# Performance work log

Measured on AMD Instinct MI355X. Metric: run time of the kernel, lower is better.

## Reference

```python
import jax, jax.numpy as jnp
import numpy as np

N_NODES = 50000
N_EDGES = 1600000
D_FEAT = 128
EMB = 32
HEADS = 4
SLOPE = 0.2  # PyG GATv2 default negative_slope


def setup_inputs() -> dict:
    key = jax.random.key(0)
    ks = jax.random.split(key, 12)
    H, C = HEADS, EMB
    hid = H * C  # concat output dim = 128

    def glorot(k, shape):
        fan_in, fan_out = shape[0], shape[-1] if len(shape) > 1 else shape[0]
        lim = jnp.sqrt(6.0 / (fan_in + fan_out)).astype(jnp.float32)
        return jax.random.uniform(k, shape, jnp.float32, -lim, lim)

    x = jax.random.normal(ks[0], (N_NODES, D_FEAT), jnp.float32)
    edge_index = jax.random.randint(ks[1], (2, N_EDGES), 0, N_NODES, jnp.int32).astype(jnp.int64)

    return {
        "x": x,
        "edge_index": edge_index,
        # layer 1: in D_FEAT -> H*C (separate source/target lins, share_weights=False)
        "W1_l": glorot(ks[2], (D_FEAT, hid)),
        "W1_r": glorot(ks[3], (D_FEAT, hid)),
        "att1": glorot(ks[4], (H, C)),
        "b1": jnp.zeros((hid,), jnp.float32),
        # layer 2: in H*C -> H*C
        "W2_l": glorot(ks[5], (hid, hid)),
        "W2_r": glorot(ks[6], (hid, hid)),
        "att2": glorot(ks[7], (H, C)),
        "b2": jnp.zeros((hid,), jnp.float32),
    }


def _gatv2_layer(x, src, dst, W_l, W_r, att, bias, n_nodes):
    H, C = att.shape
    xl = (x @ W_l).reshape(n_nodes, H, C)  # source-side transform
    xr = (x @ W_r).reshape(n_nodes, H, C)  # target-side transform
    # per-edge pre-activation: GATv2 applies LeakyReLU BEFORE the attention dot
    msg = xl[src] + xr[dst]                               # [E, H, C]
    e = jnp.einsum('ehc,hc->eh', jax.nn.leaky_relu(msg, SLOPE), att)  # [E, H]
    # numerically stable segment softmax over incoming edges of each dst node
    m = jax.ops.segment_max(e, dst, num_segments=n_nodes)  # [N, H]
    ex = jnp.exp(e - m[dst])
    denom = jax.ops.segment_sum(ex, dst, num_segments=n_nodes)  # [N, H]
    alpha = ex / (denom[dst] + 1e-16)                     # [E, H]
    out = jax.ops.segment_sum(alpha[:, :, None] * xl[src], dst, num_segments=n_nodes)
    return out.reshape(n_nodes, H * C) + bias


def reference(x, edge_index, W1_l, W1_r, att1, b1, W2_l, W2_r, att2, b2):
    n = x.shape[0]
    # PyG default add_self_loops=True: append (i -> i) for every node
    loop = jnp.arange(n, dtype=edge_index.dtype)
    src = jnp.concatenate([edge_index[0], loop])
    dst = jnp.concatenate([edge_index[1], loop])
    h = jax.nn.relu(_gatv2_layer(x, src, dst, W1_l, W1_r, att1, b1, n))
    h = jax.nn.relu(_gatv2_layer(h, src, dst, W2_l, W2_r, att2, b2, n))
    return h
```

## Files before the change

### kernel.cpp

```cpp
#include <hip/hip_runtime.h>

#define N_NODES 50000
#define N_EDGES 1600000
#define ET (N_EDGES + N_NODES)
#define DF 128
#define SLOPE 0.2f

#define NB2 391
#define CAP2 6144
#define P1_CHUNK 4096
#define GEMM_BLOCKS ((N_NODES + 63) / 64)
#define BIN_BLOCKS ((ET + P1_CHUNK - 1) / P1_CHUNK)
#define WCONV_BLOCKS 256

typedef __attribute__((ext_vector_type(4))) float floatx4;
typedef __attribute__((ext_vector_type(8))) _Float16 half8;
typedef __attribute__((ext_vector_type(2))) _Float16 half2v;

__device__ __forceinline__ void wconv_body(
    int bid,
    const float* __restrict__ W0, const float* __restrict__ W1,
    const float* __restrict__ W2, const float* __restrict__ W3,
    _Float16* __restrict__ Wh, _Float16* __restrict__ Wl)
{
    int idx = bid * 256 + threadIdx.x;
    int m = idx >> 14, rem = idx & 16383;
    const float* W = (m == 0) ? W0 : (m == 1) ? W1 : (m == 2) ? W2 : W3;
    int c = rem >> 7, k = rem & 127;
    float v = W[k * 128 + c];
    _Float16 h = (_Float16)v;
    int slab = k >> 5, q = (k >> 3) & 3, j = k & 7;
    size_t o = (size_t)m * 16384 + (size_t)((slab << 2) + q) * 1024 + (c << 3) + j;
    Wh[o] = h;
    Wl[o] = (_Float16)(v - (float)h);
}

__device__ __forceinline__ void bin_body(
    int bid, const int* __restrict__ ei,
    int* __restrict__ g_count, int* __restrict__ bucket_mem, char* smem_)
{
    int* cnt  = (int*)smem_;
    int* base = cnt + NB2;
    int* cnt2 = base + NB2;
    const int tid = threadIdx.x;

    for (int i = tid; i < NB2; i += 256) { cnt[i] = 0; cnt2[i] = 0; }
    __syncthreads();

    const int e0 = bid * P1_CHUNK;
    int srcv[16], dstv[16];
#pragma unroll
    for (int i = 0; i < 16; i++) {
        int eid = e0 + i * 256 + tid;
        int s = 0, d = -1;
        if (eid < ET) {
            if (eid < N_EDGES) { s = ei[eid]; d = ei[N_EDGES + eid]; }
            else               { s = d = eid - N_EDGES; }
        }
        srcv[i] = s; dstv[i] = d;
        if (d >= 0) atomicAdd(&cnt[d >> 7], 1);
    }
    __syncthreads();
    for (int i = tid; i < NB2; i += 256)
        base[i] = (cnt[i] > 0) ? atomicAdd(&g_count[i], cnt[i]) : 0;
    __syncthreads();
#pragma unroll
    for (int i = 0; i < 16; i++) {
        int d = dstv[i];
        if (d >= 0) {
            int b = d >> 7;
            int r = atomicAdd(&cnt2[b], 1);
            int slot = base[b] + r;
            if (slot < CAP2)
                bucket_mem[(size_t)b * CAP2 + slot] =
                    (srcv[i] & 0xFFFF) | ((d & 127) << 16);
        }
    }
}

__global__ __launch_bounds__(256) void prep_bin(
    const float* __restrict__ W0, const float* __restrict__ W1,
    const float* __restrict__ W2, const float* __restrict__ W3,
    _Float16* __restrict__ Wh, _Float16* __restrict__ Wl,
    const int* __restrict__ ei,
    int* __restrict__ g_count, int* __restrict__ bucket_mem)
{
    __shared__ char smem[4704];
    if (blockIdx.x < WCONV_BLOCKS)
        wconv_body(blockIdx.x, W0, W1, W2, W3, Wh, Wl);
    else
        bin_body(blockIdx.x - WCONV_BLOCKS, ei, g_count, bucket_mem, smem);
}

__device__ __forceinline__ half8 load_h8(const float* p) {
    float4 a = *(const float4*)(p);
    float4 b = *(const float4*)(p + 4);
    half8 h;
    h[0] = (_Float16)a.x; h[1] = (_Float16)a.y;
    h[2] = (_Float16)a.z; h[3] = (_Float16)a.w;
    h[4] = (_Float16)b.x; h[5] = (_Float16)b.y;
    h[6] = (_Float16)b.z; h[7] = (_Float16)b.w;
    return h;
}
__device__ __forceinline__ half8 load_h8(const _Float16* p) {
    return *(const half8*)p;
}

template<typename T>
__device__ __forceinline__ void gemm_body(
    int bid, const T* __restrict__ X,
    const _Float16* __restrict__ WhL, const _Float16* __restrict__ WlL,
    const _Float16* __restrict__ WhR, const _Float16* __restrict__ WlR,
    _Float16* __restrict__ outL, _Float16* __restrict__ outR, int M, char* smem_)
{
    _Float16* xs  = (_Float16*)smem_;
    _Float16* whL = xs + 64 * 40;
    _Float16* wlL = whL + 4096;
    _Float16* whR = wlL + 4096;
    _Float16* wlR = whR + 4096;

    const int t = threadIdx.x;
    const int row0 = bid * 64;
    const int lane = t & 63, wv = t >> 6;
    const int lm = lane & 15, quad = lane >> 4;
    const int m0 = wv * 16;

    floatx4 accL[8], accR[8];
#pragma unroll
    for (int i = 0; i < 8; i++) { accL[i] = (floatx4)0.f; accR[i] = (floatx4)0.f; }

    const int sr = t >> 2;
    const int sc = (t & 3) * 8;

    for (int kb = 0; kb < 128; kb += 32) {
        const int slab = kb >> 5;
        int xrow = row0 + sr; if (xrow >= M) xrow = M - 1;
        half8 xv = load_h8(X + (size_t)xrow * DF + kb + sc);
        *(half8*)&xs[sr * 40 + sc] = xv;

        {
            const size_t sbase = (size_t)slab * 4096;
            const _Float16* gsrc[4] = { WhL + sbase, WlL + sbase,
                                        WhR + sbase, WlR + sbase };
            _Float16* ldst[4] = { whL, wlL, whR, wlR };
#pragma unroll
            for (int b = 0; b < 4; b++) {
#pragma unroll
                for (int i = 0; i < 2; i++) {
                    const int chunk = wv * 2 + i;
                    const _Float16* src = gsrc[b] + chunk * 512 + lane * 8;
                    __builtin_amdgcn_global_load_lds(
                        (const __attribute__((address_space(1))) void*)src,
                        (__attribute__((address_space(3))) void*)(ldst[b] + chunk * 512),
                        16, 0, 0);
                }
            }
        }
        __syncthreads();

        half8 af = *(const half8*)&xs[(m0 + lm) * 40 + quad * 8];
#pragma unroll
        for (int nt = 0; nt < 8; nt++) {
            const int bofs = quad * 1024 + (nt * 16 + lm) * 8;
            half8 bh = *(const half8*)&whL[bofs];
            half8 bl = *(const half8*)&wlL[bofs];
            accL[nt] = __builtin_amdgcn_mfma_f32_16x16x32_f16(af, bh, accL[nt], 0, 0, 0);
            accL[nt] = __builtin_amdgcn_mfma_f32_16x16x32_f16(af, bl, accL[nt], 0, 0, 0);
            half8 ch = *(const half8*)&whR[bofs];
            half8 cl = *(const half8*)&wlR[bofs];
            accR[nt] = __builtin_amdgcn_mfma_f32_16x16x32_f16(af, ch, accR[nt], 0, 0, 0);
            accR[nt] = __builtin_amdgcn_mfma_f32_16x16x32_f16(af, cl, accR[nt], 0, 0, 0);
        }
        __syncthreads();
    }

#pragma unroll
    for (int nt = 0; nt < 8; nt++) {
        int col = (nt >> 2) * 64 + (nt & 3) * 16 + lm;
#pragma unroll
        for (int r = 0; r < 4; r++) {
            int gr = row0 + m0 + quad * 4 + r;
            if (gr < M) {
                size_t o = (size_t)gr * DF + col;
                outL[o] = (_Float16)accL[nt][r];
                outR[o] = (_Float16)accR[nt][r];
            }
        }
    }
}

__device__ __forceinline__ void csr_body(
    int b, const int* __restrict__ g_count, const int* __restrict__ bucket_mem,
    int* __restrict__ row_ptr, unsigned short* __restrict__ csr_src, char* smem_)
{
    int* sh_edges = (int*)smem_;
    int* hist = sh_edges + 6144;
    int* excl = hist + 128;
    int* cnt2 = excl + 128;
    int* sA   = cnt2 + 128;
    int* sB   = sA + 512;
    const int tid = threadIdx.x;

    sA[tid]       = (tid < NB2)       ? g_count[tid]       : 0;
    sA[tid + 256] = (tid + 256 < NB2) ? g_count[tid + 256] : 0;
    __syncthreads();
    int* in = sA; int* outp = sB;
    for (int d = 1; d < 512; d <<= 1) {
        for (int i = tid; i < 512; i += 256)
            outp[i] = in[i] + ((i >= d) ? in[i - d] : 0);
        __syncthreads();
        int* tmp = in; in = outp; outp = tmp;
    }
    const int base_csr = (b > 0) ? in[b - 1] : 0;

    int m = g_count[b]; if (m > CAP2) m = CAP2;
    if (tid < 128) { hist[tid] = 0; cnt2[tid] = 0; }
    __syncthreads();
    const int* bm = bucket_mem + (size_t)b * CAP2;
    for (int i = tid; i < m; i += 256) {
        int p = bm[i];
        sh_edges[i] = p;
        atomicAdd(&hist[(p >> 16) & 127], 1);
    }
    __syncthreads();
    if (tid < 128) sA[tid] = hist[tid];
    __syncthreads();
    for (int d = 1; d < 128; d <<= 1) {
        int x = 0;
        if (tid < 128 && tid >= d) x = sA[tid - d];
        __syncthreads();
        if (tid < 128) sA[tid] += x;
        __syncthreads();
    }
    if (tid < 128) {
        excl[tid] = sA[tid] - hist[tid];
        int node = (b << 7) + tid;
        if (node < N_NODES) row_ptr[node] = base_csr + excl[tid];
    }
    if (b == 0 && tid == 0) row_ptr[N_NODES] = ET;
    __syncthreads();
    for (int i = tid; i < m; i += 256) {
        int p = sh_edges[i];
        int dl = (p >> 16) & 127;
        int r = atomicAdd(&cnt2[dl], 1);
        csr_src[base_csr + excl[dl] + r] = (unsigned short)(p & 0xFFFF);
    }
}

__global__ __launch_bounds__(256) void gemm_csr(
    const float* __restrict__ X,
    const _Float16* __restrict__ Wh, const _Float16* __restrict__ Wl,
    _Float16* __restrict__ outL, _Float16* __restrict__ outR,
    const int* __restrict__ g_count, const int* __restrict__ bucket_mem,
    int* __restrict__ row_ptr, unsigned short* __restrict__ csr_src)
{
    __shared__ char smem[37888];
    if (blockIdx.x < GEMM_BLOCKS)
        gemm_body<float>(blockIdx.x, X, Wh, Wl, Wh + 16384, Wl + 16384,
                         outL, outR, N_NODES, smem);
    else
        csr_body(blockIdx.x - GEMM_BLOCKS, g_count, bucket_mem,
                 row_ptr, csr_src, smem);
}

__global__ __launch_bounds__(256) void gemm_f16(
    const _Float16* __restrict__ X,
    const _Float16* __restrict__ Wh, const _Float16* __restrict__ Wl,
    _Float16* __restrict__ outL, _Float16* __restrict__ outR)
{
    __shared__ char smem[37888];
    gemm_body<_Float16>(blockIdx.x, X, Wh, Wl, Wh + 16384, Wl + 16384,
                        outL, outR, N_NODES, smem);
}

template<typename TOut>
__global__ __launch_bounds__(256) void fused_agg(
    const _Float16* __restrict__ XL, const _Float16* __restrict__ XR,
    const int* __restrict__ row_ptr, const unsigned short* __restrict__ csr_src,
    const float* __restrict__ att, const float* __restrict__ bias,
    TOut* __restrict__ out)
{
    const int t = threadIdx.x;
    const int wave = t >> 6, l = t & 63;
    const int g = l >> 4, gl = l & 15;
    const int n = blockIdx.x * 4 + wave;
    if (n >= N_NODES) return;
    const int beg = row_ptr[n], end = row_ptr[n + 1];
    const int deg = end - beg;
    const int dlim = (deg < 128) ? deg : 128;

    const int liA = beg + l, liB = liA + 64;
    unsigned sa = (liA < end) ? (unsigned)csr_src[liA] : 0u;
    unsigned sb = (liB < end) ? (unsigned)csr_src[liB] : 0u;
    const unsigned s32 = sa | (sb << 16);

    const int c0 = gl * 8;
    half8 xrh = *(const half8*)(XR + (size_t)n * DF + c0);
    float4 at0 = *(const float4*)(att + c0);
    float4 at1 = *(const float4*)(att + c0 + 4);
    half2v a01 = { (_Float16)at0.x, (_Float16)at0.y };
    half2v a23 = { (_Float16)at0.z, (_Float16)at0.w };
    half2v a45 = { (_Float16)at1.x, (_Float16)at1.y };
    half2v a67 = { (_Float16)at1.z, (_Float16)at1.w };
    const half8 slp = { (_Float16)SLOPE, (_Float16)SLOPE, (_Float16)SLOPE, (_Float16)SLOPE,
                        (_Float16)SLOPE, (_Float16)SLOPE, (_Float16)SLOPE, (_Float16)SLOPE };

    float a0 = 0.f, a1 = 0.f, a2 = 0.f, a3 = 0.f;
    float a4 = 0.f, a5 = 0.f, a6 = 0.f, a7 = 0.f, den = 0.f;

#define SRC(POS)                                                               \
    ({ int _p = (POS);                                                         \
       unsigned _v = (unsigned)__shfl((int)s32, _p & 63);                      \
       (int)(((_p & 64) ? (_v >> 16) : _v) & 0xFFFFu); })
#define LDROW(S) (*(const half8*)(XL + ((size_t)(unsigned)(S) << 7) + c0))

#define EDGE_STEP(HV, EOK)                                                     \
    {                                                                          \
        const bool _ok = (EOK);                                                \
        half8 _msg = HV + xrh;                                                 \
        half8 _lk  = __builtin_elementwise_max(_msg, _msg * slp);              \
        half2v _m01 = { _lk[0], _lk[1] };                                      \
        half2v _m23 = { _lk[2], _lk[3] };                                      \
        half2v _m45 = { _lk[4], _lk[5] };                                      \
        half2v _m67 = { _lk[6], _lk[7] };                                      \
        float _sc = __builtin_amdgcn_fdot2(_m01, a01, 0.f, false);             \
        _sc = __builtin_amdgcn_fdot2(_m23, a23, _sc, false);                   \
        _sc = __builtin_amdgcn_fdot2(_m45, a45, _sc, false);                   \
        _sc = __builtin_amdgcn_fdot2(_m67, a67, _sc, false);                   \
        _sc += __shfl_xor(_sc, 1);                                             \
        _sc += __shfl_xor(_sc, 2);                                             \
        float _e = _ok ? __expf(_sc) : 0.f;                                    \
        uint4 _hw; __builtin_memcpy(&_hw, &(HV), 16);                          \
        asm("v_fma_mix_f32 %0, %1, %2, %0 op_sel:[0,0,0] op_sel_hi:[1,0,0]"    \
            : "+v"(a0) : "v"(_hw.x), "v"(_e));                                 \
        asm("v_fma_mix_f32 %0, %1, %2, %0 op_sel:[1,0,0] op_sel_hi:[1,0,0]"    \
            : "+v"(a1) : "v"(_hw.x), "v"(_e));                                 \
        asm("v_fma_mix_f32 %0, %1, %2, %0 op_sel:[0,0,0] op_sel_hi:[1,0,0]"    \
            : "+v"(a2) : "v"(_hw.y), "v"(_e));                                 \
        asm("v_fma_mix_f32 %0, %1, %2, %0 op_sel:[1,0,0] op_sel_hi:[1,0,0]"    \
            : "+v"(a3) : "v"(_hw.y), "v"(_e));                                 \
        asm("v_fma_mix_f32 %0, %1, %2, %0 op_sel:[0,0,0] op_sel_hi:[1,0,0]"    \
            : "+v"(a4) : "v"(_hw.z), "v"(_e));                                 \
        asm("v_fma_mix_f32 %0, %1, %2, %0 op_sel:[1,0,0] op_sel_hi:[1,0,0]"    \
            : "+v"(a5) : "v"(_hw.z), "v"(_e));                                 \
        asm("v_fma_mix_f32 %0, %1, %2, %0 op_sel:[0,0,0] op_sel_hi:[1,0,0]"    \
            : "+v"(a6) : "v"(_hw.w), "v"(_e));                                 \
        asm("v_fma_mix_f32 %0, %1, %2, %0 op_sel:[1,0,0] op_sel_hi:[1,0,0]"    \
            : "+v"(a7) : "v"(_hw.w), "v"(_e));                                 \
        den += _e;                                                             \
    }

    half8 X0 = LDROW(SRC(g));
    half8 X1 = LDROW(SRC(4 + g));
    half8 Y0 = LDROW(SRC(8 + g));
    half8 Y1 = LDROW(SRC(12 + g));

    int p = 0;
    for (;;) {
        EDGE_STEP(X0, (p + g < dlim))
        EDGE_STEP(X1, (p + 4 + g < dlim))
        X0 = LDROW(SRC(p + 16 + g));
        X1 = LDROW(SRC(p + 20 + g));
        p += 8;
        if (p >= dlim) break;
        EDGE_STEP(Y0, (p + g < dlim))
        EDGE_STEP(Y1, (p + 4 + g < dlim))
        Y0 = LDROW(SRC(p + 16 + g));
        Y1 = LDROW(SRC(p + 20 + g));
        p += 8;
        if (p >= dlim) break;
    }

    for (int q = 128; q < deg; q += 4) {
        int ei_ = beg + q + g;
        int s = (ei_ < end) ? (int)csr_src[ei_] : 0;
        half8 hvt = LDROW(s);
        EDGE_STEP(hvt, (q + g < deg))
    }
#undef EDGE_STEP
#undef SRC
#undef LDROW

#define CMB(x) x += __shfl_xor(x, 16); x += __shfl_xor(x, 32);
    CMB(a0) CMB(a1) CMB(a2) CMB(a3) CMB(a4) CMB(a5) CMB(a6) CMB(a7) CMB(den)
#undef CMB

    if (g == 0) {
        float inv = 1.f / (den + 1e-16f);
        float4 b0 = *(const float4*)(bias + c0);
        float4 b1 = *(const float4*)(bias + c0 + 4);
        float o[8];
        o[0] = fmaxf(a0 * inv + b0.x, 0.f);
        o[1] = fmaxf(a1 * inv + b0.y, 0.f);
        o[2] = fmaxf(a2 * inv + b0.z, 0.f);
        o[3] = fmaxf(a3 * inv + b0.w, 0.f);
        o[4] = fmaxf(a4 * inv + b1.x, 0.f);
        o[5] = fmaxf(a5 * inv + b1.y, 0.f);
        o[6] = fmaxf(a6 * inv + b1.z, 0.f);
        o[7] = fmaxf(a7 * inv + b1.w, 0.f);
        TOut* op = out + (size_t)n * DF + c0;
        if constexpr (sizeof(TOut) == 2) {
            half8 hv;
#pragma unroll
            for (int i = 0; i < 8; i++) hv[i] = (_Float16)o[i];
            *(half8*)op = hv;
        } else {
            *(float4*)(op)     = make_float4(o[0], o[1], o[2], o[3]);
            *(float4*)(op + 4) = make_float4(o[4], o[5], o[6], o[7]);
        }
    }
}

extern "C" void kernel_launch(void* const* d_in, const int* in_sizes, int n_in,
                              void* d_out, int out_size, void* d_ws, size_t ws_size,
                              hipStream_t stream)
{
    (void)in_sizes; (void)n_in; (void)out_size; (void)ws_size;

    const float* x    = (const float*)d_in[0];
    const int*   ei   = (const int*)d_in[1];
    const float* W1l  = (const float*)d_in[2];
    const float* W1r  = (const float*)d_in[3];
    const float* att1 = (const float*)d_in[4];
    const float* b1   = (const float*)d_in[5];
    const float* W2l  = (const float*)d_in[6];
    const float* W2r  = (const float*)d_in[7];
    const float* att2 = (const float*)d_in[8];
    const float* b2   = (const float*)d_in[9];
    float* out = (float*)d_out;

    char* ws = (char*)d_ws;
    size_t off = 0;
    const size_t NF = (size_t)N_NODES * DF * sizeof(float);
    _Float16* A = (_Float16*)(ws + off); off += NF / 2;
    _Float16* B = (_Float16*)(ws + off); off += NF / 2;
    _Float16* C = (_Float16*)(ws + off); off += NF / 2;
    int* bucket_mem  = (int*)(ws + off); off += (size_t)NB2 * CAP2 * sizeof(int);
    int* g_count     = (int*)(ws + off); off += 512 * sizeof(int);
    int* row_ptr     = (int*)(ws + off); off += (size_t)(N_NODES + 1) * sizeof(int);
    unsigned short* csr_src = (unsigned short*)(ws + off);
    off += ((size_t)ET * sizeof(unsigned short) + 255) & ~(size_t)255;
    _Float16* Wh = (_Float16*)(ws + off); off += 4 * 16384 * sizeof(_Float16);
    _Float16* Wl = (_Float16*)(ws + off); off += 4 * 16384 * sizeof(_Float16);

    hipMemsetAsync(g_count, 0, 512 * sizeof(int), stream);

    prep_bin<<<WCONV_BLOCKS + BIN_BLOCKS, 256, 0, stream>>>(
        W1l, W1r, W2l, W2r, Wh, Wl, ei, g_count, bucket_mem);

    gemm_csr<<<GEMM_BLOCKS + NB2, 256, 0, stream>>>(
        x, Wh, Wl, A, B, g_count, bucket_mem, row_ptr, csr_src);

    fused_agg<_Float16><<<(N_NODES + 3) / 4, 256, 0, stream>>>(
        A, B, row_ptr, csr_src, att1, b1, C);

    gemm_f16<<<GEMM_BLOCKS, 256, 0, stream>>>(C, Wh + 2 * 16384, Wl + 2 * 16384, A, B);
    fused_agg<float><<<(N_NODES + 3) / 4, 256, 0, stream>>>(
        A, B, row_ptr, csr_src, att2, b2, out);
}
```

Baseline: 267.8 us.

## Drop split-fp16 weight residual and use 512-thread 128-row GEMM tiles

Removes the hi/lo fp16 split of the weights, so the GEMM issues one MFMA per tile instead of two and loads half as much weight data into LDS. The GEMM and fused CSR kernels move to 512-thread blocks covering 128 rows each, and the CSR scan and edge loops are adjusted to the larger block. This halves matrix-core work and LDS traffic but lowers weight precision to plain fp16, which may affect accuracy.

```diff
diff --git a/kernel.cpp b/kernel.cpp
--- a/kernel.cpp
+++ b/kernel.cpp
@@ -9,7 +9,7 @@
 #define NB2 391
 #define CAP2 6144
 #define P1_CHUNK 4096
-#define GEMM_BLOCKS ((N_NODES + 63) / 64)
+#define GEMM_BLOCKS2 ((N_NODES + 127) / 128)
 #define BIN_BLOCKS ((ET + P1_CHUNK - 1) / P1_CHUNK)
 #define WCONV_BLOCKS 256
 
@@ -21,18 +21,16 @@
     int bid,
     const float* __restrict__ W0, const float* __restrict__ W1,
     const float* __restrict__ W2, const float* __restrict__ W3,
-    _Float16* __restrict__ Wh, _Float16* __restrict__ Wl)
+    _Float16* __restrict__ Wh)
 {
     int idx = bid * 256 + threadIdx.x;
     int m = idx >> 14, rem = idx & 16383;
     const float* W = (m == 0) ? W0 : (m == 1) ? W1 : (m == 2) ? W2 : W3;
     int c = rem >> 7, k = rem & 127;
     float v = W[k * 128 + c];
-    _Float16 h = (_Float16)v;
     int slab = k >> 5, q = (k >> 3) & 3, j = k & 7;
     size_t o = (size_t)m * 16384 + (size_t)((slab << 2) + q) * 1024 + (c << 3) + j;
-    Wh[o] = h;
-    Wl[o] = (_Float16)(v - (float)h);
+    Wh[o] = (_Float16)v;
 }
 
 __device__ __forceinline__ void bin_body(
@@ -81,13 +79,13 @@
 __global__ __launch_bounds__(256) void prep_bin(
     const float* __restrict__ W0, const float* __restrict__ W1,
     const float* __restrict__ W2, const float* __restrict__ W3,
-    _Float16* __restrict__ Wh, _Float16* __restrict__ Wl,
+    _Float16* __restrict__ Wh,
     const int* __restrict__ ei,
     int* __restrict__ g_count, int* __restrict__ bucket_mem)
 {
     __shared__ char smem[4704];
     if (blockIdx.x < WCONV_BLOCKS)
-        wconv_body(blockIdx.x, W0, W1, W2, W3, Wh, Wl);
+        wconv_body(blockIdx.x, W0, W1, W2, W3, Wh);
     else
         bin_body(blockIdx.x - WCONV_BLOCKS, ei, g_count, bucket_mem, smem);
 }
@@ -109,18 +107,15 @@
 template<typename T>
 __device__ __forceinline__ void gemm_body(
     int bid, const T* __restrict__ X,
-    const _Float16* __restrict__ WhL, const _Float16* __restrict__ WlL,
-    const _Float16* __restrict__ WhR, const _Float16* __restrict__ WlR,
+    const _Float16* __restrict__ WhL, const _Float16* __restrict__ WhR,
     _Float16* __restrict__ outL, _Float16* __restrict__ outR, int M, char* smem_)
 {
     _Float16* xs  = (_Float16*)smem_;
-    _Float16* whL = xs + 64 * 40;
-    _Float16* wlL = whL + 4096;
-    _Float16* whR = wlL + 4096;
-    _Float16* wlR = whR + 4096;
+    _Float16* whL = xs + 128 * 40;
+    _Float16* whR = whL + 4096;
 
     const int t = threadIdx.x;
-    const int row0 = bid * 64;
+    const int row0 = bid * 128;
     const int lane = t & 63, wv = t >> 6;
     const int lm = lane & 15, quad = lane >> 4;
     const int m0 = wv * 16;
@@ -139,22 +134,15 @@
         *(half8*)&xs[sr * 40 + sc] = xv;
 
         {
-            const size_t sbase = (size_t)slab * 4096;
-            const _Float16* gsrc[4] = { WhL + sbase, WlL + sbase,
-                                        WhR + sbase, WlR + sbase };
-            _Float16* ldst[4] = { whL, wlL, whR, wlR };
-#pragma unroll
-            for (int b = 0; b < 4; b++) {
-#pragma unroll
-                for (int i = 0; i < 2; i++) {
-                    const int chunk = wv * 2 + i;
-                    const _Float16* src = gsrc[b] + chunk * 512 + lane * 8;
-                    __builtin_amdgcn_global_load_lds(
-                        (const __attribute__((address_space(1))) void*)src,
-                        (__attribute__((address_space(3))) void*)(ldst[b] + chunk * 512),
-                        16, 0, 0);
-                }
-            }
+            const size_t sbase = (size_t)slab * 4096 + wv * 512 + lane * 8;
+            __builtin_amdgcn_global_load_lds(
+                (const __attribute__((address_space(1))) void*)(WhL + sbase),
+                (__attribute__((address_space(3))) void*)(whL + wv * 512),
+                16, 0, 0);
+            __builtin_amdgcn_global_load_lds(
+                (const __attribute__((address_space(1))) void*)(WhR + sbase),
+                (__attribute__((address_space(3))) void*)(whR + wv * 512),
+                16, 0, 0);
         }
         __syncthreads();
 
@@ -163,13 +151,9 @@
         for (int nt = 0; nt < 8; nt++) {
             const int bofs = quad * 1024 + (nt * 16 + lm) * 8;
             half8 bh = *(const half8*)&whL[bofs];
-            half8 bl = *(const half8*)&wlL[bofs];
             accL[nt] = __builtin_amdgcn_mfma_f32_16x16x32_f16(af, bh, accL[nt], 0, 0, 0);
-            accL[nt] = __builtin_amdgcn_mfma_f32_16x16x32_f16(af, bl, accL[nt], 0, 0, 0);
             half8 ch = *(const half8*)&whR[bofs];
-            half8 cl = *(const half8*)&wlR[bofs];
             accR[nt] = __builtin_amdgcn_mfma_f32_16x16x32_f16(af, ch, accR[nt], 0, 0, 0);
-            accR[nt] = __builtin_amdgcn_mfma_f32_16x16x32_f16(af, cl, accR[nt], 0, 0, 0);
         }
         __syncthreads();
     }
@@ -201,13 +185,11 @@
     int* sB   = sA + 512;
     const int tid = threadIdx.x;
 
-    sA[tid]       = (tid < NB2)       ? g_count[tid]       : 0;
-    sA[tid + 256] = (tid + 256 < NB2) ? g_count[tid + 256] : 0;
+    sA[tid] = (tid < NB2) ? g_count[tid] : 0;
     __syncthreads();
     int* in = sA; int* outp = sB;
     for (int d = 1; d < 512; d <<= 1) {
-        for (int i = tid; i < 512; i += 256)
-            outp[i] = in[i] + ((i >= d) ? in[i - d] : 0);
+        outp[tid] = in[tid] + ((tid >= d) ? in[tid - d] : 0);
         __syncthreads();
         int* tmp = in; in = outp; outp = tmp;
     }
@@ -217,7 +199,7 @@
     if (tid < 128) { hist[tid] = 0; cnt2[tid] = 0; }
     __syncthreads();
     const int* bm = bucket_mem + (size_t)b * CAP2;
-    for (int i = tid; i < m; i += 256) {
+    for (int i = tid; i < m; i += 512) {
         int p = bm[i];
         sh_edges[i] = p;
         atomicAdd(&hist[(p >> 16) & 127], 1);
@@ -239,7 +221,7 @@
     }
     if (b == 0 && tid == 0) row_ptr[N_NODES] = ET;
     __syncthreads();
-    for (int i = tid; i < m; i += 256) {
+    for (int i = tid; i < m; i += 512) {
         int p = sh_edges[i];
         int dl = (p >> 16) & 127;
         int r = atomicAdd(&cnt2[dl], 1);
@@ -247,30 +229,28 @@
     }
 }
 
-__global__ __launch_bounds__(256) void gemm_csr(
+__global__ __launch_bounds__(512) void gemm_csr(
     const float* __restrict__ X,
-    const _Float16* __restrict__ Wh, const _Float16* __restrict__ Wl,
+    const _Float16* __restrict__ WhL, const _Float16* __restrict__ WhR,
     _Float16* __restrict__ outL, _Float16* __restrict__ outR,
     const int* __restrict__ g_count, const int* __restrict__ bucket_mem,
     int* __restrict__ row_ptr, unsigned short* __restrict__ csr_src)
 {
-    __shared__ char smem[37888];
-    if (blockIdx.x < GEMM_BLOCKS)
-        gemm_body<float>(blockIdx.x, X, Wh, Wl, Wh + 16384, Wl + 16384,
-                         outL, outR, N_NODES, smem);
+    __shared__ char smem[30720];
+    if (blockIdx.x < GEMM_BLOCKS2)
+        gemm_body<float>(blockIdx.x, X, WhL, WhR, outL, outR, N_NODES, smem);
     else
-        csr_body(blockIdx.x - GEMM_BLOCKS, g_count, bucket_mem,
+        csr_body(blockIdx.x - GEMM_BLOCKS2, g_count, bucket_mem,
                  row_ptr, csr_src, smem);
 }
 
-__global__ __launch_bounds__(256) void gemm_f16(
+__global__ __launch_bounds__(512) void gemm_f16(
     const _Float16* __restrict__ X,
-    const _Float16* __restrict__ Wh, const _Float16* __restrict__ Wl,
+    const _Float16* __restrict__ WhL, const _Float16* __restrict__ WhR,
     _Float16* __restrict__ outL, _Float16* __restrict__ outR)
 {
-    __shared__ char smem[37888];
-    gemm_body<_Float16>(blockIdx.x, X, Wh, Wl, Wh + 16384, Wl + 16384,
-                        outL, outR, N_NODES, smem);
+    __shared__ char smem[30720];
+    gemm_body<_Float16>(blockIdx.x, X, WhL, WhR, outL, outR, N_NODES, smem);
 }
 
 template<typename TOut>
@@ -441,20 +421,20 @@
     unsigned short* csr_src = (unsigned short*)(ws + off);
     off += ((size_t)ET * sizeof(unsigned short) + 255) & ~(size_t)255;
     _Float16* Wh = (_Float16*)(ws + off); off += 4 * 16384 * sizeof(_Float16);
-    _Float16* Wl = (_Float16*)(ws + off); off += 4 * 16384 * sizeof(_Float16);
 
     hipMemsetAsync(g_count, 0, 512 * sizeof(int), stream);
 
     prep_bin<<<WCONV_BLOCKS + BIN_BLOCKS, 256, 0, stream>>>(
-        W1l, W1r, W2l, W2r, Wh, Wl, ei, g_count, bucket_mem);
-
-    gemm_csr<<<GEMM_BLOCKS + NB2, 256, 0, stream>>>(
-        x, Wh, Wl, A, B, g_count, bucket_mem, row_ptr, csr_src);
+        W1l, W1r, W2l, W2r, Wh, ei, g_count, bucket_mem);
+
+    gemm_csr<<<GEMM_BLOCKS2 + NB2, 512, 0, stream>>>(
+        x, Wh, Wh + 16384, A, B, g_count, bucket_mem, row_ptr, csr_src);
 
     fused_agg<_Float16><<<(N_NODES + 3) / 4, 256, 0, stream>>>(
         A, B, row_ptr, csr_src, att1, b1, C);
 
-    gemm_f16<<<GEMM_BLOCKS, 256, 0, stream>>>(C, Wh + 2 * 16384, Wl + 2 * 16384, A, B);
+    gemm_f16<<<GEMM_BLOCKS2, 512, 0, stream>>>(
+        C, Wh + 2 * 16384, Wh + 3 * 16384, A, B);
     fused_agg<float><<<(N_NODES + 3) / 4, 256, 0, stream>>>(
         A, B, row_ptr, csr_src, att2, b2, out);
 }
```

Measured after the change: 256.4 us. 1.04x faster.
